# Performance work log

Hardware: AMD Instinct MI355X
Metric: run time of the kernel (lower is better)

The kernel has to match this reference:

```python
import jax, jax.numpy as jnp
import numpy as np

C = 512
G = 32  # groups
EPS = 1e-6

def setup_inputs() -> dict:
    key = jax.random.key(0)
    ks = jax.random.split(key, 12)
    x = jax.random.normal(ks[0], (2, C, 64, 64), dtype=jnp.float32)
    s = 1.0 / np.sqrt(C)
    params = {
        'gn_scale': jnp.ones((C,), jnp.float32),
        'gn_bias': jnp.zeros((C,), jnp.float32),
        'wq': jax.random.normal(ks[1], (C, C), jnp.float32) * s,
        'bq': jax.random.normal(ks[2], (C,), jnp.float32) * 0.01,
        'wk': jax.random.normal(ks[3], (C, C), jnp.float32) * s,
        'bk': jax.random.normal(ks[4], (C,), jnp.float32) * 0.01,
        'wv': jax.random.normal(ks[5], (C, C), jnp.float32) * s,
        'bv': jax.random.normal(ks[6], (C,), jnp.float32) * 0.01,
        'wp': jax.random.normal(ks[7], (C, C), jnp.float32) * s,
        'bp': jax.random.normal(ks[8], (C,), jnp.float32) * 0.01,
    }
    return {'x': x, **params}


def _group_norm(x, scale, bias):
    b, c, h, w = x.shape
    xg = x.reshape(b, G, c // G, h, w)
    mean = jnp.mean(xg, axis=(2, 3, 4), keepdims=True)
    var = jnp.var(xg, axis=(2, 3, 4), keepdims=True)
    xg = (xg - mean) * jax.lax.rsqrt(var + EPS)
    x = xg.reshape(b, c, h, w)
    return x * scale[None, :, None, None] + bias[None, :, None, None]


def _conv1x1(x, w, bias):
    # x: [b,c,h,w], w: [out,in] -> [b,out,h,w]
    return jnp.einsum('oc,bchw->bohw', w, x) + bias[None, :, None, None]


def reference(x, gn_scale, gn_bias, wq, bq, wk, bk, wv, bv, wp, bp):
    h = _group_norm(x, gn_scale, gn_bias)
    q = _conv1x1(h, wq, bq)
    k = _conv1x1(h, wk, bk)
    v = _conv1x1(h, wv, bv)
    b, c, h_, w_ = q.shape
    n = h_ * w_
    q = q.reshape(b, c, n)
    k = k.reshape(b, c, n)
    v = v.reshape(b, c, n)
    # attn[b,i,j] = sum_c q[b,c,i] k[b,c,j] * c^-0.5
    attn = jnp.einsum('bci,bcj->bij', q, k) * (c ** -0.5)
    attn = jax.nn.softmax(attn, axis=2)
    # out[b,c,i] = sum_j v[b,c,j] attn[b,i,j]
    out = jnp.einsum('bcj,bij->bci', v, attn)
    out = out.reshape(b, c, h_, w_)
    out = _conv1x1(out, wp, bp)
    return x + out
```

## Files before the change

kernel.cpp:

```cpp
#include <hip/hip_runtime.h>
#include <stdint.h>

typedef short short8 __attribute__((ext_vector_type(8)));
typedef short short4v __attribute__((ext_vector_type(4)));
typedef float f32x4 __attribute__((ext_vector_type(4)));
typedef float float4v __attribute__((ext_vector_type(4)));

__device__ inline float bf2f(short s) {
    union { unsigned u; float f; } c;
    c.u = ((unsigned)(unsigned short)s) << 16;
    return c.f;
}
__device__ inline short f2bf(float f) {
    union { float f; unsigned u; } c;
    c.f = f;
    unsigned u = c.u;
    unsigned r = (u + 0x7fffu + ((u >> 16) & 1u)) >> 16;
    return (short)r;
}

typedef const __attribute__((address_space(1))) char GChar;
typedef __attribute__((address_space(3))) char LChar;
__device__ __forceinline__ void gload_lds16(const void* g, void* l) {
    __builtin_amdgcn_global_load_lds((GChar*)g, (LChar*)l, 16, 0, 0);
}

template<int N> __device__ __forceinline__ void wait_vm() {
    if constexpr (N == 0)      asm volatile("s_waitcnt vmcnt(0)" ::: "memory");
    else if constexpr (N == 4) asm volatile("s_waitcnt vmcnt(4)" ::: "memory");
    else if constexpr (N == 6) asm volatile("s_waitcnt vmcnt(6)" ::: "memory");
    else static_assert(N == 0 || N == 4 || N == 6, "unsupported vmcnt");
}

__device__ __forceinline__ void wait_lgkm0() {
    asm volatile("s_waitcnt lgkmcnt(0)" ::: "memory");
}
__device__ __forceinline__ void wait_lgkm8() {
    asm volatile("s_waitcnt lgkmcnt(8)" ::: "memory");
}

__device__ __forceinline__ void phase_barrier() {
    __builtin_amdgcn_s_barrier();
    asm volatile("" ::: "memory");
}

__device__ __forceinline__ void swz_xy(int& bx, int& by) {
    int gx = gridDim.x;
    int nwg = gx * gridDim.y;
    int wg = by * gx + bx;
    int chunk = nwg >> 3;
    int swz = (wg & 7) * chunk + (wg >> 3);
    bx = swz % gx;
    by = swz / gx;
}

__global__ __launch_bounds__(256) void conv_w4(const float* __restrict__ w0, const float* __restrict__ w1,
                                               const float* __restrict__ w2, const float* __restrict__ w3,
                                               short* __restrict__ dst, float s0,
                                               float* __restrict__ rowsum) {
    if (blockIdx.x < 32) rowsum[blockIdx.x * 256 + threadIdx.x] = 0.0f;
    int idx = (blockIdx.x * 256 + threadIdx.x) * 4;
    int wi = idx >> 18;
    int off = idx & 262143;
    const float* src = (wi == 0) ? w0 : (wi == 1) ? w1 : (wi == 2) ? w2 : w3;
    float sc = (wi == 0) ? s0 : 1.0f;
    float4v v = *reinterpret_cast<const float4v*>(src + off);
    short4v o;
    o[0] = f2bf(v[0] * sc); o[1] = f2bf(v[1] * sc);
    o[2] = f2bf(v[2] * sc); o[3] = f2bf(v[3] * sc);
    *reinterpret_cast<short4v*>(dst + idx) = o;
}

__global__ __launch_bounds__(256) void prep_bias(const float* __restrict__ bq, const float* __restrict__ bk,
                                                 float* __restrict__ bqk, float s,
                                                 float* __restrict__ statsraw) {
    int i = blockIdx.x * 256 + threadIdx.x;
    if (i < 128) statsraw[i] = 0.0f;
    bqk[i] = (i < 512) ? bq[i] * s : bk[i - 512];
}

__global__ __launch_bounds__(256) void gn_stats2(const float* __restrict__ x, float* __restrict__ statsraw) {
    int bg = blockIdx.x;
    const float* p = x + (size_t)bg * 65536 + blockIdx.y * 8192;
    float s = 0.f, ss = 0.f;
    #pragma unroll
    for (int i = threadIdx.x * 4; i < 8192; i += 1024) {
        float4v q = *reinterpret_cast<const float4v*>(p + i);
        s  += q[0] + q[1] + q[2] + q[3];
        ss += q[0]*q[0] + q[1]*q[1] + q[2]*q[2] + q[3]*q[3];
    }
    #pragma unroll
    for (int off = 32; off >= 1; off >>= 1) {
        s  += __shfl_xor(s, off);
        ss += __shfl_xor(ss, off);
    }
    __shared__ float rs[8];
    int w = threadIdx.x >> 6, lane = threadIdx.x & 63;
    if (lane == 0) { rs[w] = s; rs[4 + w] = ss; }
    __syncthreads();
    if (threadIdx.x == 0) {
        float S1 = rs[0] + rs[1] + rs[2] + rs[3];
        float S2 = rs[4] + rs[5] + rs[6] + rs[7];
        atomicAdd(&statsraw[bg * 2],     S1);
        atomicAdd(&statsraw[bg * 2 + 1], S2);
    }
}

__global__ __launch_bounds__(256) void gn_apply_t(const float* __restrict__ x, const float* __restrict__ statsraw,
                                                  const float* __restrict__ scale, const float* __restrict__ bias,
                                                  short* __restrict__ hT) {
    __shared__ float t[64][65];
    int n0 = blockIdx.x * 64, c0 = blockIdx.y * 64, b = blockIdx.z;
    const float* xb = x + (size_t)b * 512 * 4096;
    int col = threadIdx.x & 63, rb = threadIdx.x >> 6;
    #pragma unroll
    for (int r = 0; r < 16; ++r) {
        int cl = rb + r * 4;
        int c = c0 + cl;
        int g = c >> 4;
        float sum   = statsraw[(b * 32 + g) * 2];
        float sumsq = statsraw[(b * 32 + g) * 2 + 1];
        float mean = sum * (1.f / 65536.f);
        float var  = sumsq * (1.f / 65536.f) - mean * mean;
        float rstd = rsqrtf(var + 1e-6f);
        float v = xb[(size_t)c * 4096 + n0 + col];
        t[col][cl] = (v - mean) * rstd * scale[c] + bias[c];
    }
    __syncthreads();
    short* hb = hT + (size_t)b * 4096 * 512;
    #pragma unroll
    for (int r = 0; r < 16; ++r) {
        int nl = rb + r * 4;
        hb[(size_t)(n0 + nl) * 512 + c0 + col] = f2bf(t[nl][col]);
    }
}

template<int EPI>
__global__ __launch_bounds__(512, 2) void gemm8b(
    const short* __restrict__ A, int zdiv, long sAb1, long sAb2, int lda,
    const short* __restrict__ B, long sBb1, long sBb2, int ldb,
    short* __restrict__ C, long sCb1, long sCb2, int ldc,
    int K, float* __restrict__ rowsum)
{
    __shared__ __align__(16) char lds[131072];

    const int tid = threadIdx.x;
    int bx = blockIdx.x, by = blockIdx.y;
    swz_xy(bx, by);
    const int bm = bx * 256, bn = by * 256;
    const int zb = blockIdx.z / zdiv, zs = blockIdx.z % zdiv;

    const short* Ab = A + (size_t)zb * sAb1 + (size_t)zs * sAb2;
    const short* Bb = B + (size_t)zb * sBb1 + (size_t)zs * sBb2;

    const int w = tid >> 6, lane = tid & 63;
    const int wm = w >> 2, wn = w & 3;
    const int l15 = lane & 15, l4 = lane >> 4;

    long srcAh[2][2], srcBh[2][2]; int dstAh[2][2], dstBh[2][2];
    #pragma unroll
    for (int h = 0; h < 2; ++h) {
        #pragma unroll
        for (int i = 0; i < 2; ++i) {
            int ch = i * 512 + tid;
            int r = h * 128 + (ch >> 3), c = ch & 7;
            srcAh[h][i] = (long)(bm + r) * lda + ((c ^ (r & 7)) << 3);
            dstAh[h][i] = r * 128 + c * 16;
            srcBh[h][i] = (long)(bn + r) * ldb + ((c ^ (r & 7)) << 3);
            dstBh[h][i] = 32768 + r * 128 + c * 16;
        }
    }
    auto stageAh = [&](int buf, int h, long kt) {
        char* l = lds + buf * 65536;
        gload_lds16(Ab + srcAh[h][0] + kt, l + dstAh[h][0]);
        gload_lds16(Ab + srcAh[h][1] + kt, l + dstAh[h][1]);
    };
    auto stageBh = [&](int buf, int h, long kt) {
        char* l = lds + buf * 65536;
        gload_lds16(Bb + srcBh[h][0] + kt, l + dstBh[h][0]);
        gload_lds16(Bb + srcBh[h][1] + kt, l + dstBh[h][1]);
    };

    auto fragA = [&](const char* base, int m, int ks) -> short8 {
        int r = wm * 128 + m * 16 + l15;
        int kk = ks * 4 + l4;
        return *reinterpret_cast<const short8*>(base + r * 128 + ((kk * 16) ^ ((r & 7) << 4)));
    };
    auto fragB = [&](const char* base, int n, int ks) -> short8 {
        int r = wn * 64 + n * 16 + l15;
        int kk = ks * 4 + l4;
        return *reinterpret_cast<const short8*>(base + 32768 + r * 128 + ((kk * 16) ^ ((r & 7) << 4)));
    };

    f32x4 acc[8][4] = {};
    const int nk = K >> 6;

    stageBh(0, 0, 0); stageBh(0, 1, 0);
    stageAh(0, 0, 0); stageAh(0, 1, 0);
    if (nk > 1) {
        stageBh(1, 0, 64); stageBh(1, 1, 64);
        wait_vm<4>();
    } else {
        wait_vm<0>();
    }
    phase_barrier();

    short8 bf[4][2];

    for (int t = 0; t < nk; ++t) {
        const char* lr = lds + (t & 1) * 65536;
        const int bufN = (t & 1) ^ 1;
        const int bufT = (t & 1);
        const long ktA = (long)(t + 1) << 6;
        const long ktB = (long)(t + 2) << 6;
        const bool pA = (t + 1 < nk);
        const bool pB = (t + 2 < nk);
        short8 a00, a01, a10, a11;

        #pragma unroll
        for (int n = 0; n < 4; ++n) { bf[n][0] = fragB(lr, n, 0); bf[n][1] = fragB(lr, n, 1); }
        a00 = fragA(lr, 0, 0); a01 = fragA(lr, 0, 1);
        a10 = fragA(lr, 1, 0); a11 = fragA(lr, 1, 1);
        if (pA) stageAh(bufN, 0, ktA);
        wait_lgkm8();
        phase_barrier();
        wait_lgkm0();
        __builtin_amdgcn_s_setprio(1);
        #pragma unroll
        for (int n = 0; n < 4; ++n) {
            acc[0][n] = __builtin_amdgcn_mfma_f32_16x16x32_bf16(a00, bf[n][0], acc[0][n], 0, 0, 0);
            acc[0][n] = __builtin_amdgcn_mfma_f32_16x16x32_bf16(a01, bf[n][1], acc[0][n], 0, 0, 0);
            acc[1][n] = __builtin_amdgcn_mfma_f32_16x16x32_bf16(a10, bf[n][0], acc[1][n], 0, 0, 0);
            acc[1][n] = __builtin_amdgcn_mfma_f32_16x16x32_bf16(a11, bf[n][1], acc[1][n], 0, 0, 0);
        }
        __builtin_amdgcn_s_setprio(0);
        __builtin_amdgcn_sched_barrier(0);
        phase_barrier();

        a00 = fragA(lr, 2, 0); a01 = fragA(lr, 2, 1);
        a10 = fragA(lr, 3, 0); a11 = fragA(lr, 3, 1);
        if (pA) stageAh(bufN, 1, ktA);
        phase_barrier();
        wait_lgkm0();
        __builtin_amdgcn_s_setprio(1);
        #pragma unroll
        for (int n = 0; n < 4; ++n) {
            acc[2][n] = __builtin_amdgcn_mfma_f32_16x16x32_bf16(a00, bf[n][0], acc[2][n], 0, 0, 0);
            acc[2][n] = __builtin_amdgcn_mfma_f32_16x16x32_bf16(a01, bf[n][1], acc[2][n], 0, 0, 0);
            acc[3][n] = __builtin_amdgcn_mfma_f32_16x16x32_bf16(a10, bf[n][0], acc[3][n], 0, 0, 0);
            acc[3][n] = __builtin_amdgcn_mfma_f32_16x16x32_bf16(a11, bf[n][1], acc[3][n], 0, 0, 0);
        }
        __builtin_amdgcn_s_setprio(0);
        __builtin_amdgcn_sched_barrier(0);
        phase_barrier();

        a00 = fragA(lr, 4, 0); a01 = fragA(lr, 4, 1);
        a10 = fragA(lr, 5, 0); a11 = fragA(lr, 5, 1);
        if (pB) stageBh(bufT, 0, ktB);
        phase_barrier();
        wait_lgkm0();
        __builtin_amdgcn_s_setprio(1);
        #pragma unroll
        for (int n = 0; n < 4; ++n) {
            acc[4][n] = __builtin_amdgcn_mfma_f32_16x16x32_bf16(a00, bf[n][0], acc[4][n], 0, 0, 0);
            acc[4][n] = __builtin_amdgcn_mfma_f32_16x16x32_bf16(a01, bf[n][1], acc[4][n], 0, 0, 0);
            acc[5][n] = __builtin_amdgcn_mfma_f32_16x16x32_bf16(a10, bf[n][0], acc[5][n], 0, 0, 0);
            acc[5][n] = __builtin_amdgcn_mfma_f32_16x16x32_bf16(a11, bf[n][1], acc[5][n], 0, 0, 0);
        }
        __builtin_amdgcn_s_setprio(0);
        __builtin_amdgcn_sched_barrier(0);
        phase_barrier();

        a00 = fragA(lr, 6, 0); a01 = fragA(lr, 6, 1);
        a10 = fragA(lr, 7, 0); a11 = fragA(lr, 7, 1);
        if (pB) stageBh(bufT, 1, ktB);
        if (pB)      wait_vm<4>();
        else if (pA) wait_vm<0>();
        phase_barrier();
        wait_lgkm0();
        __builtin_amdgcn_s_setprio(1);
        #pragma unroll
        for (int n = 0; n < 4; ++n) {
            acc[6][n] = __builtin_amdgcn_mfma_f32_16x16x32_bf16(a00, bf[n][0], acc[6][n], 0, 0, 0);
            acc[6][n] = __builtin_amdgcn_mfma_f32_16x16x32_bf16(a01, bf[n][1], acc[6][n], 0, 0, 0);
            acc[7][n] = __builtin_amdgcn_mfma_f32_16x16x32_bf16(a10, bf[n][0], acc[7][n], 0, 0, 0);
            acc[7][n] = __builtin_amdgcn_mfma_f32_16x16x32_bf16(a11, bf[n][1], acc[7][n], 0, 0, 0);
        }
        __builtin_amdgcn_s_setprio(0);
        __builtin_amdgcn_sched_barrier(0);
        phase_barrier();
    }

    short* Cb = C + (size_t)zb * sCb1 + (size_t)zs * sCb2;
    if constexpr (EPI == 0) {
        #pragma unroll
        for (int m = 0; m < 8; ++m) {
            #pragma unroll
            for (int r = 0; r < 4; ++r) {
                int row = bm + wm * 128 + m * 16 + l4 * 4 + r;
                #pragma unroll
                for (int n = 0; n < 4; ++n) {
                    int col = bn + wn * 64 + n * 16 + l15;
                    Cb[(size_t)row * ldc + col] = f2bf(acc[m][n][r]);
                }
            }
        }
    } else {
        float* lsum = (float*)lds;
        #pragma unroll
        for (int m = 0; m < 8; ++m) {
            #pragma unroll
            for (int r = 0; r < 4; ++r) {
                int lrow = wm * 128 + m * 16 + l4 * 4 + r;
                int row = bm + lrow;
                float part = 0.0f;
                #pragma unroll
                for (int n = 0; n < 4; ++n) {
                    int col = bn + wn * 64 + n * 16 + l15;
                    float e = __expf(acc[m][n][r]);
                    part += e;
                    Cb[(size_t)row * ldc + col] = f2bf(e);
                }
                part += __shfl_xor(part, 1);
                part += __shfl_xor(part, 2);
                part += __shfl_xor(part, 4);
                part += __shfl_xor(part, 8);
                if (l15 == 0) lsum[wn * 256 + lrow] = part;
            }
        }
        __syncthreads();
        if (tid < 256) {
            float s = (lsum[tid] + lsum[256 + tid]) + (lsum[512 + tid] + lsum[768 + tid]);
            atomicAdd(&rowsum[zb * 4096 + bm + tid], s);
        }
    }
}

template<int BMT, int BNT, int WM, int WN>
__global__ __launch_bounds__(512) void gemm_nt3(
    const short* __restrict__ A, int zdiv, long sAb1, long sAb2, int lda,
    const short* __restrict__ B, long sBb1, long sBb2, int ldb,
    void* __restrict__ Cv, long sCb1, long sCb2, int ldc,
    int K,
    const float* __restrict__ bias, int bias_mode,
    const float* __restrict__ res, long sResb,
    int c_fp32)
{
    constexpr int BUFB = (BMT + BNT) * 128;
    constexpr int ALPT = BMT / 64;
    constexpr int BLPT = BNT / 64;
    constexpr int MF   = BMT / WM / 16;
    constexpr int NF   = BNT / WN / 16;
    __shared__ __align__(16) char lds[2 * BUFB];

    const int tid = threadIdx.x;
    int bx = blockIdx.x, by = blockIdx.y;
    swz_xy(bx, by);
    const int bm = bx * BMT;
    const int bn = by * BNT;
    const int bz = blockIdx.z;
    const int zb = bz / zdiv, zs = bz % zdiv;

    const short* Ab = A + (size_t)zb * sAb1 + (size_t)zs * sAb2;
    const short* Bb = B + (size_t)zb * sBb1 + (size_t)zs * sBb2;

    const int w = tid >> 6;
    const int lane = tid & 63;
    const int wm = w / WN, wn = w % WN;
    const int wr = wm * (BMT / WM);
    const int wc = wn * (BNT / WN);

    f32x4 acc[MF][NF] = {};
    const int nk = K >> 6;

    auto stage = [&](int buf, int kt) {
        char* la = lds + buf * BUFB;
        char* lb = la + BMT * 128;
        #pragma unroll
        for (int i = 0; i < ALPT; ++i) {
            int ch = i * 512 + tid;
            int r = ch >> 3, c = ch & 7;
            gload_lds16(Ab + (size_t)(bm + r) * lda + kt + ((c ^ (r & 7)) << 3), la + ch * 16);
        }
        #pragma unroll
        for (int i = 0; i < BLPT; ++i) {
            int ch = i * 512 + tid;
            int r = ch >> 3, c = ch & 7;
            gload_lds16(Bb + (size_t)(bn + r) * ldb + kt + ((c ^ (r & 7)) << 3), lb + ch * 16);
        }
    };

    stage(0, 0);
    int cur = 0;
    for (int t = 0; t < nk; ++t) {
        if (t + 1 < nk) {
            stage(cur ^ 1, (t + 1) << 6);
            wait_vm<6>();
        } else {
            wait_vm<0>();
        }
        phase_barrier();

        const char* la = lds + cur * BUFB;
        const char* lb = la + BMT * 128;
        #pragma unroll
        for (int ks = 0; ks < 2; ++ks) {
            const int kb = ks * 64 + (lane >> 4) * 16;
            short8 af[MF], bfv[NF];
            #pragma unroll
            for (int m = 0; m < MF; ++m) {
                int r = wr + m * 16 + (lane & 15);
                af[m] = *reinterpret_cast<const short8*>(la + r * 128 + (kb ^ ((r & 7) << 4)));
            }
            #pragma unroll
            for (int n = 0; n < NF; ++n) {
                int r = wc + n * 16 + (lane & 15);
                bfv[n] = *reinterpret_cast<const short8*>(lb + r * 128 + (kb ^ ((r & 7) << 4)));
            }
            #pragma unroll
            for (int m = 0; m < MF; ++m)
                #pragma unroll
                for (int n = 0; n < NF; ++n)
                    acc[m][n] = __builtin_amdgcn_mfma_f32_16x16x32_bf16(af[m], bfv[n], acc[m][n], 0, 0, 0);
        }
        asm volatile("" ::: "memory");
        __builtin_amdgcn_s_barrier();
        cur ^= 1;
    }

    const int row0 = (lane >> 4) * 4;
    const int col0 = lane & 15;
    short* Cb16 = (short*)Cv + (size_t)zb * sCb1 + (size_t)zs * sCb2;
    float* Cf32 = (float*)Cv + (size_t)zb * sCb1 + (size_t)zs * sCb2;
    const float* resb = res ? res + (size_t)zb * sResb : nullptr;

    #pragma unroll
    for (int m = 0; m < MF; ++m) {
        #pragma unroll
        for (int r = 0; r < 4; ++r) {
            int row = bm + wr + m * 16 + row0 + r;
            float bvr = (bias_mode == 1) ? bias[row] : 0.0f;
            #pragma unroll
            for (int n = 0; n < NF; ++n) {
                int col = bn + wc + n * 16 + col0;
                float v = acc[m][n][r];
                if (bias_mode == 1) v += bvr;
                else if (bias_mode == 2) v += bias[col];
                size_t idx = (size_t)row * ldc + col;
                if (c_fp32) {
                    if (resb) v += resb[idx];
                    Cf32[idx] = v;
                } else {
                    Cb16[idx] = f2bf(v);
                }
            }
        }
    }
}

template<int BNT>
__global__ __launch_bounds__(256) void gemm_nt2(
    const short* __restrict__ A, long sAb, int lda,
    const short* __restrict__ B, long sBb, int ldb,
    void* __restrict__ Cv, long sCb, int ldc,
    int K,
    const float* __restrict__ bias, int bias_mode,
    const float* __restrict__ res, long sResb,
    int c_fp32)
{
    constexpr int BMT = 128;
    constexpr int NF  = BNT / 32;
    constexpr int BUF = (BMT + BNT) * 128;
    constexpr int ALPT = (BMT * 8) / 256;
    constexpr int BLPT = (BNT * 8) / 256;
    __shared__ __align__(16) char lds[2 * BUF];

    const int tid = threadIdx.x;
    int bx = blockIdx.x, by = blockIdx.y;
    swz_xy(bx, by);
    const int bm = bx * BMT;
    const int bn = by * BNT;
    const int bz = blockIdx.z;

    const short* Ab = A + (size_t)bz * sAb;
    const short* Bb = B + (size_t)bz * sBb;

    const int w = tid >> 6;
    const int lane = tid & 63;
    const int wr = (w >> 1) * 64;
    const int wc = (w & 1) * (BNT / 2);

    f32x4 acc[4][NF] = {};
    const int nk = K >> 6;

    auto stage = [&](int buf, int kt) {
        char* la = lds + buf * BUF;
        char* lb = la + BMT * 128;
        #pragma unroll
        for (int i = 0; i < ALPT; ++i) {
            int ch = i * 256 + tid;
            int r = ch >> 3, c = ch & 7;
            gload_lds16(Ab + (size_t)(bm + r) * lda + kt + ((c ^ (r & 7)) << 3), la + ch * 16);
        }
        #pragma unroll
        for (int i = 0; i < BLPT; ++i) {
            int ch = i * 256 + tid;
            int r = ch >> 3, c = ch & 7;
            gload_lds16(Bb + (size_t)(bn + r) * ldb + kt + ((c ^ (r & 7)) << 3), lb + ch * 16);
        }
    };

    stage(0, 0);
    int cur = 0;
    for (int t = 0; t < nk; ++t) {
        if (t + 1 < nk) {
            stage(cur ^ 1, (t + 1) << 6);
            wait_vm<6>();
        } else {
            wait_vm<0>();
        }
        phase_barrier();

        const char* la = lds + cur * BUF;
        const char* lb = la + BMT * 128;
        #pragma unroll
        for (int ks = 0; ks < 2; ++ks) {
            const int kb = ks * 64 + (lane >> 4) * 16;
            short8 af[4], bfv[NF];
            #pragma unroll
            for (int m = 0; m < 4; ++m) {
                int r = wr + m * 16 + (lane & 15);
                af[m] = *reinterpret_cast<const short8*>(la + r * 128 + (kb ^ ((r & 7) << 4)));
            }
            #pragma unroll
            for (int n = 0; n < NF; ++n) {
                int r = wc + n * 16 + (lane & 15);
                bfv[n] = *reinterpret_cast<const short8*>(lb + r * 128 + (kb ^ ((r & 7) << 4)));
            }
            #pragma unroll
            for (int m = 0; m < 4; ++m)
                #pragma unroll
                for (int n = 0; n < NF; ++n)
                    acc[m][n] = __builtin_amdgcn_mfma_f32_16x16x32_bf16(af[m], bfv[n], acc[m][n], 0, 0, 0);
        }
        asm volatile("" ::: "memory");
        __builtin_amdgcn_s_barrier();
        cur ^= 1;
    }

    const int row0 = (lane >> 4) * 4;
    const int col0 = lane & 15;
    short* Cb16 = (short*)Cv + (size_t)bz * sCb;
    float* Cf32 = (float*)Cv + (size_t)bz * sCb;
    const float* resb = res ? res + (size_t)bz * sResb : nullptr;

    #pragma unroll
    for (int m = 0; m < 4; ++m) {
        #pragma unroll
        for (int r = 0; r < 4; ++r) {
            int row = bm + wr + m * 16 + row0 + r;
            float bvr = (bias_mode == 1) ? bias[row] : 0.0f;
            #pragma unroll
            for (int n = 0; n < NF; ++n) {
                int col = bn + wc + n * 16 + col0;
                float v = acc[m][n][r];
                if (bias_mode == 1) v += bvr;
                else if (bias_mode == 2) v += bias[col];
                size_t idx = (size_t)row * ldc + col;
                if (c_fp32) {
                    if (resb) v += resb[idx];
                    Cf32[idx] = v;
                } else {
                    Cb16[idx] = f2bf(v);
                }
            }
        }
    }
}

__global__ __launch_bounds__(256) void reduce4b(const short* __restrict__ p, short* __restrict__ o,
                                                const float* __restrict__ rowsum) {
    const long NN = 4096L * 512L;
    const short* pb = p + (size_t)blockIdx.y * 4 * NN;
    short* ob = o + (size_t)blockIdx.y * NN;
    const float* rs = rowsum + (size_t)blockIdx.y * 4096;
    long i = (blockIdx.x * 256 + threadIdx.x) * 8L;
    int row = (int)(i >> 9);
    float inv = 1.0f / rs[row];
    short8 a = *reinterpret_cast<const short8*>(pb + i);
    short8 b = *reinterpret_cast<const short8*>(pb + NN + i);
    short8 c = *reinterpret_cast<const short8*>(pb + 2 * NN + i);
    short8 d = *reinterpret_cast<const short8*>(pb + 3 * NN + i);
    short8 r;
    #pragma unroll
    for (int j = 0; j < 8; ++j)
        r[j] = f2bf(((bf2f(a[j]) + bf2f(b[j])) + (bf2f(c[j]) + bf2f(d[j]))) * inv);
    *reinterpret_cast<short8*>(ob + i) = r;
}

extern "C" void kernel_launch(void* const* d_in, const int* in_sizes, int n_in,
                              void* d_out, int out_size, void* d_ws, size_t ws_size,
                              hipStream_t stream) {
    (void)in_sizes; (void)n_in; (void)out_size; (void)ws_size;
    const float* x        = (const float*)d_in[0];
    const float* gn_scale = (const float*)d_in[1];
    const float* gn_bias  = (const float*)d_in[2];
    const float* wq = (const float*)d_in[3];
    const float* bq = (const float*)d_in[4];
    const float* wk = (const float*)d_in[5];
    const float* bk = (const float*)d_in[6];
    const float* wv = (const float*)d_in[7];
    const float* bv = (const float*)d_in[8];
    const float* wp = (const float*)d_in[9];
    const float* bp = (const float*)d_in[10];

    char* ws = (char*)d_ws;
    const size_t MB = 1024 * 1024;
    short* hT   = (short*)(ws + 0);
    short* QKT  = (short*)(ws + 8   * MB);
    short* V    = (short*)(ws + 24  * MB);
    short* OT   = (short*)(ws + 32  * MB);
    short* S    = (short*)(ws + 40  * MB);
    short* part = (short*)(ws + 104 * MB);
    short* wB   = (short*)(ws + 168 * MB);
    float* statsraw = (float*)(ws + 170 * MB);
    float* bqk  = (float*)(ws + 170 * MB + 4096);
    float* rowsum = (float*)(ws + 171 * MB);

    const long NC   = 4096L * 512L;
    const long CN   = 512L * 4096L;
    const long QKNC = 4096L * 1024L;
    const long SNN  = 4096L * 4096L;
    const float attn_scale = 0.044194173824159216f;

    conv_w4<<<1024, 256, 0, stream>>>(wq, wk, wv, wp, wB, attn_scale, rowsum);
    prep_bias<<<4, 256, 0, stream>>>(bq, bk, bqk, attn_scale, statsraw);

    gn_stats2<<<dim3(64, 8), 256, 0, stream>>>(x, statsraw);
    gn_apply_t<<<dim3(64, 8, 2), 256, 0, stream>>>(x, statsraw, gn_scale, gn_bias, hT);

    gemm_nt3<128, 256, 2, 4><<<dim3(32, 4, 2), 512, 0, stream>>>(
        hT, 1, NC, 0, 512, wB, 0, 0, 512, QKT, QKNC, 0, 1024, 512, bqk, 2, nullptr, 0, 0);
    gemm_nt2<64><<<dim3(4, 64, 2), 256, 0, stream>>>(
        wB + 524288, 0, 512, hT, NC, 512, V, CN, 4096, 512, bv, 1, nullptr, 0, 0);

    gemm8b<1><<<dim3(16, 16, 2), 512, 0, stream>>>(
        QKT, 1, QKNC, 0, 1024, QKT + 512, QKNC, 0, 1024, S, SNN, 0, 4096, 512, rowsum);
    gemm8b<0><<<dim3(16, 2, 8), 512, 0, stream>>>(
        S, 4, SNN, 1024, 4096, V, CN, 1024, 4096, part, 4L * NC, NC, 512, 1024, nullptr);
    reduce4b<<<dim3(1024, 2), 256, 0, stream>>>(part, OT, rowsum);

    gemm_nt2<64><<<dim3(4, 64, 2), 256, 0, stream>>>(
        wB + 786432, 0, 512, OT, NC, 512, d_out, CN, 4096, 512, bp, 1, x, CN, 1);
}
```

Measured before the change: 172.1 us.

## Fuse split-K reduction into output projection and fold bias prep into weight conversion

```diff
diff --git a/kernel.cpp b/kernel.cpp
--- a/kernel.cpp
+++ b/kernel.cpp
@@ -57,9 +57,14 @@
 __global__ __launch_bounds__(256) void conv_w4(const float* __restrict__ w0, const float* __restrict__ w1,
                                                const float* __restrict__ w2, const float* __restrict__ w3,
                                                short* __restrict__ dst, float s0,
-                                               float* __restrict__ rowsum) {
-    if (blockIdx.x < 32) rowsum[blockIdx.x * 256 + threadIdx.x] = 0.0f;
-    int idx = (blockIdx.x * 256 + threadIdx.x) * 4;
+                                               float* __restrict__ rowsum,
+                                               const float* __restrict__ bq, const float* __restrict__ bk,
+                                               float* __restrict__ bqk, float* __restrict__ statsraw) {
+    int gid = blockIdx.x * 256 + threadIdx.x;
+    if (gid < 8192) rowsum[gid] = 0.0f;
+    if (gid < 128)  statsraw[gid] = 0.0f;
+    if (gid < 1024) bqk[gid] = (gid < 512) ? bq[gid] * s0 : bk[gid - 512];
+    int idx = gid * 4;
     int wi = idx >> 18;
     int off = idx & 262143;
     const float* src = (wi == 0) ? w0 : (wi == 1) ? w1 : (wi == 2) ? w2 : w3;
@@ -69,14 +74,6 @@
     o[0] = f2bf(v[0] * sc); o[1] = f2bf(v[1] * sc);
     o[2] = f2bf(v[2] * sc); o[3] = f2bf(v[3] * sc);
     *reinterpret_cast<short4v*>(dst + idx) = o;
-}
-
-__global__ __launch_bounds__(256) void prep_bias(const float* __restrict__ bq, const float* __restrict__ bk,
-                                                 float* __restrict__ bqk, float s,
-                                                 float* __restrict__ statsraw) {
-    int i = blockIdx.x * 256 + threadIdx.x;
-    if (i < 128) statsraw[i] = 0.0f;
-    bqk[i] = (i < 512) ? bq[i] * s : bk[i - 512];
 }
 
 __global__ __launch_bounds__(256) void gn_stats2(const float* __restrict__ x, float* __restrict__ statsraw) {
@@ -302,6 +299,20 @@
                 for (int n = 0; n < 4; ++n) {
                     int col = bn + wn * 64 + n * 16 + l15;
                     Cb[(size_t)row * ldc + col] = f2bf(acc[m][n][r]);
+                }
+            }
+        }
+    } else if constexpr (EPI == 2) {
+        #pragma unroll
+        for (int m = 0; m < 8; ++m) {
+            #pragma unroll
+            for (int r = 0; r < 4; ++r) {
+                int row = bm + wm * 128 + m * 16 + l4 * 4 + r;
+                float inv = 1.0f / rowsum[zb * 4096 + row];
+                #pragma unroll
+                for (int n = 0; n < 4; ++n) {
+                    int col = bn + wn * 64 + n * 16 + l15;
+                    Cb[(size_t)row * ldc + col] = f2bf(acc[m][n][r] * inv);
                 }
             }
         }
@@ -578,24 +589,135 @@
     }
 }
 
-__global__ __launch_bounds__(256) void reduce4b(const short* __restrict__ p, short* __restrict__ o,
-                                                const float* __restrict__ rowsum) {
-    const long NN = 4096L * 512L;
-    const short* pb = p + (size_t)blockIdx.y * 4 * NN;
-    short* ob = o + (size_t)blockIdx.y * NN;
-    const float* rs = rowsum + (size_t)blockIdx.y * 4096;
-    long i = (blockIdx.x * 256 + threadIdx.x) * 8L;
-    int row = (int)(i >> 9);
-    float inv = 1.0f / rs[row];
-    short8 a = *reinterpret_cast<const short8*>(pb + i);
-    short8 b = *reinterpret_cast<const short8*>(pb + NN + i);
-    short8 c = *reinterpret_cast<const short8*>(pb + 2 * NN + i);
-    short8 d = *reinterpret_cast<const short8*>(pb + 3 * NN + i);
-    short8 r;
-    #pragma unroll
-    for (int j = 0; j < 8; ++j)
-        r[j] = f2bf(((bf2f(a[j]) + bf2f(b[j])) + (bf2f(c[j]) + bf2f(d[j]))) * inv);
-    *reinterpret_cast<short8*>(ob + i) = r;
+__global__ __launch_bounds__(256) void gemm_out(
+    const short* __restrict__ A,
+    const short* __restrict__ part, long sPz, long sPb,
+    float* __restrict__ Cout, long sCb, int ldc,
+    const float* __restrict__ bias,
+    const float* __restrict__ res, long sResb)
+{
+    constexpr int BMT = 128, BNT = 64;
+    constexpr int BUF = (BMT + BNT) * 128;
+    __shared__ __align__(16) char lds[2 * BUF];
+
+    const int tid = threadIdx.x;
+    int bx = blockIdx.x, by = blockIdx.y;
+    swz_xy(bx, by);
+    const int bm = bx * BMT;
+    const int bn = by * BNT;
+    const int bz = blockIdx.z;
+
+    const short* Pb = part + (size_t)bz * sPb;
+
+    const int w = tid >> 6;
+    const int lane = tid & 63;
+    const int wr = (w >> 1) * 64;
+    const int wc = (w & 1) * 32;
+
+    f32x4 acc[4][2] = {};
+    const int nk = 8;
+
+    long srcA[4]; int dstA[4];
+    #pragma unroll
+    for (int i = 0; i < 4; ++i) {
+        int ch = i * 256 + tid;
+        int r = ch >> 3, c = ch & 7;
+        srcA[i] = (long)(bm + r) * 512 + ((c ^ (r & 7)) << 3);
+        dstA[i] = ch * 16;
+    }
+    long srcB[2]; int dstB[2];
+    #pragma unroll
+    for (int i = 0; i < 2; ++i) {
+        int ch = i * 256 + tid;
+        int r = ch >> 3, c = ch & 7;
+        srcB[i] = (long)(bn + r) * 512 + c * 8;
+        dstB[i] = BMT * 128 + r * 128 + ((c * 16) ^ ((r & 7) << 4));
+    }
+
+    auto stageA = [&](int buf, long kt) {
+        char* la = lds + buf * BUF;
+        #pragma unroll
+        for (int i = 0; i < 4; ++i) gload_lds16(A + srcA[i] + kt, la + dstA[i]);
+    };
+    auto loadB = [&](long kt, short8 rv[2][4]) {
+        #pragma unroll
+        for (int i = 0; i < 2; ++i)
+            #pragma unroll
+            for (int z = 0; z < 4; ++z)
+                rv[i][z] = *reinterpret_cast<const short8*>(Pb + z * sPz + srcB[i] + kt);
+    };
+    auto writeB = [&](int buf, short8 rv[2][4]) {
+        char* l = lds + buf * BUF;
+        #pragma unroll
+        for (int i = 0; i < 2; ++i) {
+            short8 o;
+            #pragma unroll
+            for (int j = 0; j < 8; ++j)
+                o[j] = f2bf((bf2f(rv[i][0][j]) + bf2f(rv[i][1][j])) +
+                            (bf2f(rv[i][2][j]) + bf2f(rv[i][3][j])));
+            *reinterpret_cast<short8*>(l + dstB[i]) = o;
+        }
+    };
+
+    short8 rv[2][4];
+    stageA(0, 0);
+    loadB(0, rv);
+    writeB(0, rv);
+    __syncthreads();
+
+    int cur = 0;
+    for (int t = 0; t < nk; ++t) {
+        const bool pA = (t + 1 < nk);
+        if (pA) {
+            stageA(cur ^ 1, (long)(t + 1) << 6);
+            loadB((long)(t + 1) << 6, rv);
+        }
+        const char* la = lds + cur * BUF;
+        const char* lb = la + BMT * 128;
+        #pragma unroll
+        for (int ks = 0; ks < 2; ++ks) {
+            const int kb = ks * 64 + (lane >> 4) * 16;
+            short8 af[4], bfv[2];
+            #pragma unroll
+            for (int m = 0; m < 4; ++m) {
+                int r = wr + m * 16 + (lane & 15);
+                af[m] = *reinterpret_cast<const short8*>(la + r * 128 + (kb ^ ((r & 7) << 4)));
+            }
+            #pragma unroll
+            for (int n = 0; n < 2; ++n) {
+                int r = wc + n * 16 + (lane & 15);
+                bfv[n] = *reinterpret_cast<const short8*>(lb + r * 128 + (kb ^ ((r & 7) << 4)));
+            }
+            #pragma unroll
+            for (int m = 0; m < 4; ++m)
+                #pragma unroll
+                for (int n = 0; n < 2; ++n)
+                    acc[m][n] = __builtin_amdgcn_mfma_f32_16x16x32_bf16(af[m], bfv[n], acc[m][n], 0, 0, 0);
+        }
+        if (pA) writeB(cur ^ 1, rv);
+        __syncthreads();
+        cur ^= 1;
+    }
+
+    const int row0 = (lane >> 4) * 4;
+    const int col0 = lane & 15;
+    float* Cb = Cout + (size_t)bz * sCb;
+    const float* resb = res + (size_t)bz * sResb;
+
+    #pragma unroll
+    for (int m = 0; m < 4; ++m) {
+        #pragma unroll
+        for (int r = 0; r < 4; ++r) {
+            int row = bm + wr + m * 16 + row0 + r;
+            float bvr = bias[row];
+            #pragma unroll
+            for (int n = 0; n < 2; ++n) {
+                int col = bn + wc + n * 16 + col0;
+                size_t idx = (size_t)row * ldc + col;
+                Cb[idx] = acc[m][n][r] + bvr + resb[idx];
+            }
+        }
+    }
 }
 
 extern "C" void kernel_launch(void* const* d_in, const int* in_sizes, int n_in,
@@ -619,7 +741,6 @@
     short* hT   = (short*)(ws + 0);
     short* QKT  = (short*)(ws + 8   * MB);
     short* V    = (short*)(ws + 24  * MB);
-    short* OT   = (short*)(ws + 32  * MB);
     short* S    = (short*)(ws + 40  * MB);
     short* part = (short*)(ws + 104 * MB);
     short* wB   = (short*)(ws + 168 * MB);
@@ -633,8 +754,8 @@
     const long SNN  = 4096L * 4096L;
     const float attn_scale = 0.044194173824159216f;
 
-    conv_w4<<<1024, 256, 0, stream>>>(wq, wk, wv, wp, wB, attn_scale, rowsum);
-    prep_bias<<<4, 256, 0, stream>>>(bq, bk, bqk, attn_scale, statsraw);
+    conv_w4<<<1024, 256, 0, stream>>>(wq, wk, wv, wp, wB, attn_scale, rowsum,
+                                      bq, bk, bqk, statsraw);
 
     gn_stats2<<<dim3(64, 8), 256, 0, stream>>>(x, statsraw);
     gn_apply_t<<<dim3(64, 8, 2), 256, 0, stream>>>(x, statsraw, gn_scale, gn_bias, hT);
@@ -646,10 +767,9 @@
 
     gemm8b<1><<<dim3(16, 16, 2), 512, 0, stream>>>(
         QKT, 1, QKNC, 0, 1024, QKT + 512, QKNC, 0, 1024, S, SNN, 0, 4096, 512, rowsum);
-    gemm8b<0><<<dim3(16, 2, 8), 512, 0, stream>>>(
-        S, 4, SNN, 1024, 4096, V, CN, 1024, 4096, part, 4L * NC, NC, 512, 1024, nullptr);
-    reduce4b<<<dim3(1024, 2), 256, 0, stream>>>(part, OT, rowsum);
-
-    gemm_nt2<64><<<dim3(4, 64, 2), 256, 0, stream>>>(
-        wB + 786432, 0, 512, OT, NC, 512, d_out, CN, 4096, 512, bp, 1, x, CN, 1);
-}
+    gemm8b<2><<<dim3(16, 2, 8), 512, 0, stream>>>(
+        S, 4, SNN, 1024, 4096, V, CN, 1024, 4096, part, 4L * NC, NC, 512, 1024, rowsum);
+
+    gemm_out<<<dim3(4, 64, 2), 256, 0, stream>>>(
+        wB + 786432, part, NC, 4L * NC, (float*)d_out, CN, 4096, bp, x, CN);
+}
```

New measurement: 156.2 us, median of 2. -9.2%, faster.
